# Kernel tuning notes

Hardware: AMD Instinct MI355X
Metric: run time of the kernel (lower is better)

The kernel has to match this reference:

```python
import jax, jax.numpy as jnp
import numpy as np

N_HEAD = 16
N_EMBD = 2048
HEAD_DIM = N_EMBD // N_HEAD


def setup_inputs() -> dict:
    key = jax.random.key(0)
    kx, kqkv, kp = jax.random.split(key, 3)
    B, S = 2, 2048
    x = jax.random.normal(kx, (B, S, N_EMBD), dtype=jnp.float32)
    # torch nn.Linear weights, stored as [out, in]; y = x @ W.T
    scale = 1.0 / np.sqrt(N_EMBD)
    Wqkv = jax.random.uniform(kqkv, (3 * N_EMBD, N_EMBD), dtype=jnp.float32, minval=-scale, maxval=scale)
    Wproj = jax.random.uniform(kp, (N_EMBD, N_EMBD), dtype=jnp.float32, minval=-scale, maxval=scale)
    return {"x": x, "Wqkv": Wqkv, "Wproj": Wproj}


def reference(x, Wqkv, Wproj):
    B, S, E = x.shape
    qkv = x @ Wqkv.T  # [B,S,3E]
    q, k, v = jnp.split(qkv, 3, axis=2)
    # [B,H,S,D]
    q = q.reshape(B, S, N_HEAD, HEAD_DIM).transpose(0, 2, 1, 3)
    k = k.reshape(B, S, N_HEAD, HEAD_DIM).transpose(0, 2, 1, 3)
    v = v.reshape(B, S, N_HEAD, HEAD_DIM).transpose(0, 2, 1, 3)
    scores = jnp.einsum('bhqd,bhkd->bhqk', q, k) / jnp.sqrt(jnp.float32(HEAD_DIM))
    causal = jnp.tril(jnp.ones((S, S), dtype=bool))  # [S,S]
    scores = jnp.where(causal[None, None, :, :], scores, -jnp.inf)
    weights = jax.nn.softmax(scores, axis=-1)
    out = jnp.einsum('bhqk,bhkd->bhqd', weights, v)  # [B,H,S,D]
    out = out.transpose(0, 2, 1, 3).reshape(B, S, E)
    return out @ Wproj.T
```

## Files before the change

### kernel.cpp

```cpp
#include <hip/hip_runtime.h>
#include <cstdint>
#include <cstddef>

typedef __bf16 bf16;
typedef __bf16 bf16x8 __attribute__((ext_vector_type(8)));
typedef float  f32x4  __attribute__((ext_vector_type(4)));

static_assert(sizeof(bf16x8) == 16, "bf16x8 must be 16B");

__device__ __forceinline__ void async_copy16(const bf16* g, bf16* l) {
  __builtin_amdgcn_global_load_lds(
      (__attribute__((address_space(1))) void*)(g),
      (__attribute__((address_space(3))) void*)(l),
      16, 0, 0);
}

__global__ __launch_bounds__(256)
void conv_f32_bf16(const float* __restrict__ s, bf16* __restrict__ d) {
  const size_t i = ((size_t)blockIdx.x * 256 + threadIdx.x) * 8;
  const f32x4 a = *(const f32x4*)(s + i);
  const f32x4 b = *(const f32x4*)(s + i + 4);
  bf16x8 o;
#pragma unroll
  for (int e = 0; e < 4; ++e) { o[e] = (bf16)a[e]; o[4 + e] = (bf16)b[e]; }
  *(bf16x8*)(d + i) = o;
}

template<int AMODE, int CMODE>
__global__ __launch_bounds__(256, 2)
void gemm_bt(const bf16* __restrict__ A, const bf16* __restrict__ W,
             float* __restrict__ Crow, bf16* __restrict__ Cq,
             bf16* __restrict__ Ck, bf16* __restrict__ Cvt,
             int M, int N, int K, int nbase) {
  __shared__ bf16 As[128 * 64];
  __shared__ bf16 Ws[128 * 64];

  const int tid  = threadIdx.x;
  const int wave = tid >> 6;
  const int lane = tid & 63;
  const int quad = lane >> 4;
  const int r    = lane & 15;
  const int m0 = blockIdx.y * 128;
  const int n0 = blockIdx.x * 128;
  const int wm = (wave >> 1) * 64;
  const int wn = (wave & 1) * 64;

  const int lrow   = lane >> 3;
  const int gchunk = (lane & 7) ^ lrow;

  f32x4 acc[4][4] = {};

  for (int k0 = 0; k0 < K; k0 += 64) {
    __syncthreads();
    for (int j = 0; j < 4; ++j) {
      const int rbase = (wave * 4 + j) * 8;
      const int rowA  = m0 + rbase + lrow;
      const bf16* aSrc;
      if constexpr (AMODE == 2) {
        const int b = rowA >> 11, s = rowA & 2047;
        aSrc = A + ((size_t)(b * 16 + (k0 >> 7)) * 2048 + s) * 128
                 + (k0 & 127) + gchunk * 8;
      } else {
        aSrc = A + (size_t)rowA * K + k0 + gchunk * 8;
      }
      async_copy16(aSrc, As + rbase * 64);
      async_copy16(W + (size_t)(n0 + rbase + lrow) * K + k0 + gchunk * 8,
                   Ws + rbase * 64);
    }
    __syncthreads();
    for (int ks = 0; ks < 2; ++ks) {
      bf16x8 af[4], bfv[4];
      for (int i = 0; i < 4; ++i) {
        const int ar = wm + i * 16 + r;
        af[i]  = *(const bf16x8*)(As + ar * 64 + (((ks * 4 + quad) ^ (ar & 7)) * 8));
        const int br = wn + i * 16 + r;
        bfv[i] = *(const bf16x8*)(Ws + br * 64 + (((ks * 4 + quad) ^ (br & 7)) * 8));
      }
      for (int i = 0; i < 4; ++i)
        for (int j = 0; j < 4; ++j)
          acc[i][j] = __builtin_amdgcn_mfma_f32_16x16x32_bf16(af[i], bfv[j], acc[i][j], 0, 0, 0);
    }
  }

  for (int i = 0; i < 4; ++i) {
    const int growb = m0 + wm + i * 16 + quad * 4;
    for (int j = 0; j < 4; ++j) {
      const int gcol = n0 + wn + j * 16 + r;
      for (int rg = 0; rg < 4; ++rg) {
        const int grow = growb + rg;
        if constexpr (CMODE == 1) {
          const int gc = nbase + gcol;
          const int which = gc >> 11;
          const int h = (gc >> 7) & 15;
          const int d = gc & 127;
          const int b = grow >> 11;
          const int s = grow & 2047;
          const bf16 v = (bf16)acc[i][j][rg];
          if (which == 0)
            Cq[(((size_t)b * 16 + h) * 2048 + s) * 128 + d] = v;
          else if (which == 1)
            Ck[(((size_t)b * 16 + h) * 2048 + s) * 128 + d] = v;
          else
            Cvt[(((size_t)b * 16 + h) * 128 + d) * 2048 + s] = v;
        } else {
          Crow[(size_t)grow * N + gcol] = acc[i][j][rg];
        }
      }
    }
  }
}

__global__ __launch_bounds__(256, 2)
void attn_kernel(bf16* __restrict__ Q, const bf16* __restrict__ K,
                 const bf16* __restrict__ Vt, int S) {
  __shared__ bf16 k_lds[64 * 128];
  __shared__ bf16 v_lds[128 * 64];
  __shared__ bf16 p_lds[4][32 * 64];

  const int tid = threadIdx.x, wave = tid >> 6, lane = tid & 63;
  const int quad = lane >> 4, r = lane & 15;
  const int bh = blockIdx.y;
  const int q0 = (gridDim.x - 1 - blockIdx.x) * 128;
  const int qrow0 = q0 + wave * 32;
  bf16* Qh = Q + (size_t)bh * S * 128;
  const bf16* Kh = K + (size_t)bh * S * 128;
  const bf16* Vth = Vt + (size_t)bh * 128 * S;

  bf16x8 qf[2][4];
  for (int mt = 0; mt < 2; ++mt)
    for (int ks = 0; ks < 4; ++ks)
      qf[mt][ks] = *(const bf16x8*)(Qh + (size_t)(qrow0 + mt * 16 + r) * 128 + ks * 32 + quad * 8);

  f32x4 o_acc[2][8] = {};
  f32x4 m_run[2], l_run[2];
  for (int mt = 0; mt < 2; ++mt)
    for (int t = 0; t < 4; ++t) { m_run[mt][t] = -1e30f; l_run[mt][t] = 0.f; }

  const float sc = 0.0883883476483184f * 1.4426950408889634f;
  const int nkv = (q0 + 128) >> 6;

  for (int kt = 0; kt < nkv; ++kt) {
    const int kv0 = kt << 6;
    __syncthreads();
    for (int j = 0; j < 4; ++j) {
      const int lin = j * 256 + tid;
      const int row = lin >> 4;
      const int ch  = lin & 15;
      *(bf16x8*)(k_lds + row * 128 + (ch ^ (row & 7)) * 8) =
          *(const bf16x8*)(Kh + (size_t)(kv0 + row) * 128 + ch * 8);
    }
    for (int j = 0; j < 4; ++j) {
      const int lin = j * 256 + tid;
      const int row = lin >> 3;
      const int c   = lin & 7;
      *(bf16x8*)(v_lds + row * 64 + (c ^ (row & 7)) * 8) =
          *(const bf16x8*)(Vth + (size_t)row * S + kv0 + c * 8);
    }
    __syncthreads();

    if (kv0 <= qrow0 + 31) {
      f32x4 sa[2][4] = {};
      for (int ks = 0; ks < 4; ++ks) {
        bf16x8 kf[4];
        for (int nt = 0; nt < 4; ++nt) {
          const int kr = nt * 16 + r;
          kf[nt] = *(const bf16x8*)(k_lds + kr * 128 + (((ks * 4 + quad) ^ (kr & 7)) * 8));
        }
        for (int mt = 0; mt < 2; ++mt)
          for (int nt = 0; nt < 4; ++nt)
            sa[mt][nt] = __builtin_amdgcn_mfma_f32_16x16x32_bf16(qf[mt][ks], kf[nt], sa[mt][nt], 0, 0, 0);
      }
      if (kv0 + 63 > qrow0) {
        for (int mt = 0; mt < 2; ++mt)
          for (int nt = 0; nt < 4; ++nt) {
            const int col  = kv0 + nt * 16 + r;
            const int rowb = qrow0 + mt * 16 + quad * 4;
            for (int rg = 0; rg < 4; ++rg)
              if (col > rowb + rg) sa[mt][nt][rg] = -1e30f;
          }
      }
      for (int mt = 0; mt < 2; ++mt) {
        f32x4 mx = sa[mt][0];
        for (int nt = 1; nt < 4; ++nt)
          for (int rg = 0; rg < 4; ++rg) mx[rg] = fmaxf(mx[rg], sa[mt][nt][rg]);
        for (int off = 1; off < 16; off <<= 1)
          for (int rg = 0; rg < 4; ++rg) mx[rg] = fmaxf(mx[rg], __shfl_xor(mx[rg], off, 64));
        f32x4 alpha;
        for (int rg = 0; rg < 4; ++rg) {
          const float mnew = fmaxf(m_run[mt][rg], mx[rg]);
          alpha[rg] = exp2f((m_run[mt][rg] - mnew) * sc);
          m_run[mt][rg] = mnew;
        }
        f32x4 rsum = {0.f, 0.f, 0.f, 0.f};
        for (int nt = 0; nt < 4; ++nt)
          for (int rg = 0; rg < 4; ++rg) {
            const float p = exp2f((sa[mt][nt][rg] - m_run[mt][rg]) * sc);
            sa[mt][nt][rg] = p;
            rsum[rg] += p;
          }
        for (int off = 1; off < 16; off <<= 1)
          for (int rg = 0; rg < 4; ++rg) rsum[rg] += __shfl_xor(rsum[rg], off, 64);
        for (int rg = 0; rg < 4; ++rg) l_run[mt][rg] = l_run[mt][rg] * alpha[rg] + rsum[rg];
        for (int nt2 = 0; nt2 < 8; ++nt2)
          for (int rg = 0; rg < 4; ++rg) o_acc[mt][nt2][rg] *= alpha[rg];
        for (int nt = 0; nt < 4; ++nt)
          for (int rg = 0; rg < 4; ++rg) {
            const int prow = mt * 16 + quad * 4 + rg;
            const int pcol = nt * 16 + r;
            p_lds[wave][prow * 64 + (((pcol >> 3) ^ (prow & 7)) * 8) + (pcol & 7)] =
                (bf16)sa[mt][nt][rg];
          }
      }
      for (int ks2 = 0; ks2 < 2; ++ks2) {
        bf16x8 pf[2];
        for (int mt = 0; mt < 2; ++mt) {
          const int prow = mt * 16 + r;
          pf[mt] = *(const bf16x8*)(p_lds[wave] + prow * 64 + (((ks2 * 4 + quad) ^ (prow & 7)) * 8));
        }
        for (int nt2 = 0; nt2 < 8; ++nt2) {
          const int vrow = nt2 * 16 + r;
          const bf16x8 vf = *(const bf16x8*)(v_lds + vrow * 64 + (((ks2 * 4 + quad) ^ (vrow & 7)) * 8));
          for (int mt = 0; mt < 2; ++mt)
            o_acc[mt][nt2] = __builtin_amdgcn_mfma_f32_16x16x32_bf16(pf[mt], vf, o_acc[mt][nt2], 0, 0, 0);
        }
      }
    }
  }

  for (int mt = 0; mt < 2; ++mt) {
    f32x4 inv;
    for (int rg = 0; rg < 4; ++rg) inv[rg] = 1.0f / l_run[mt][rg];
    for (int nt2 = 0; nt2 < 8; ++nt2) {
      const int d = nt2 * 16 + r;
      for (int rg = 0; rg < 4; ++rg) {
        const int s = qrow0 + mt * 16 + quad * 4 + rg;
        Qh[(size_t)s * 128 + d] = (bf16)(o_acc[mt][nt2][rg] * inv[rg]);
      }
    }
  }
}

extern "C" void kernel_launch(void* const* d_in, const int* in_sizes, int n_in,
                              void* d_out, int out_size, void* d_ws, size_t ws_size,
                              hipStream_t stream) {
  const float* x     = (const float*)d_in[0];
  const float* Wqkv  = (const float*)d_in[1];
  const float* Wproj = (const float*)d_in[2];
  float* out = (float*)d_out;

  const int Bm = 4096, E = 2048;
  const size_t plane = 8388608;

  bf16* qw  = (bf16*)d_ws;
  bf16* vtw = qw + plane;
  bf16* xb  = vtw + plane;
  bf16* kw  = (bf16*)d_out;
  bf16* wqb = kw + plane;

  conv_f32_bf16<<<8388608 / 2048, 256, 0, stream>>>(x, xb);
  conv_f32_bf16<<<6291456 / 2048, 256, 0, stream>>>(Wqkv, wqb);
  gemm_bt<0, 1><<<dim3(3072 / 128, Bm / 128), 256, 0, stream>>>(
      xb, wqb, nullptr, qw, kw, vtw, Bm, 3072, E, 0);
  conv_f32_bf16<<<6291456 / 2048, 256, 0, stream>>>(Wqkv + 6291456, wqb);
  gemm_bt<0, 1><<<dim3(3072 / 128, Bm / 128), 256, 0, stream>>>(
      xb, wqb, nullptr, qw, kw, vtw, Bm, 3072, E, 3072);
  attn_kernel<<<dim3(2048 / 128, 32), 256, 0, stream>>>(qw, kw, vtw, 2048);
  conv_f32_bf16<<<4194304 / 2048, 256, 0, stream>>>(Wproj, xb);
  gemm_bt<2, 0><<<dim3(2048 / 128, Bm / 128), 256, 0, stream>>>(
      qw, xb, out, nullptr, nullptr, nullptr, Bm, 2048, E, 0);
}
```

Before: 443.2 us.

## Shrink attention query tile to 64 rows, one 16-row MFMA tile per wave

The attention kernel now processes 64 query rows per block instead of 128, with each wave owning a single 16-row tile. This halves per-wave accumulator registers, allows a launch bound of four blocks per CU, doubles the grid and gives finer causal load balance. The cost is that each K/V tile staged in LDS is reused by half as many query rows, which roughly doubles K/V global loads and LDS staging per unit of work.

```diff
diff --git a/kernel.cpp b/kernel.cpp
--- a/kernel.cpp
+++ b/kernel.cpp
@@ -110,34 +110,32 @@
   }
 }
 
-__global__ __launch_bounds__(256, 2)
+__global__ __launch_bounds__(256, 4)
 void attn_kernel(bf16* __restrict__ Q, const bf16* __restrict__ K,
                  const bf16* __restrict__ Vt, int S) {
   __shared__ bf16 k_lds[64 * 128];
   __shared__ bf16 v_lds[128 * 64];
-  __shared__ bf16 p_lds[4][32 * 64];
+  __shared__ bf16 p_lds[4][16 * 64];
 
   const int tid = threadIdx.x, wave = tid >> 6, lane = tid & 63;
   const int quad = lane >> 4, r = lane & 15;
   const int bh = blockIdx.y;
-  const int q0 = (gridDim.x - 1 - blockIdx.x) * 128;
-  const int qrow0 = q0 + wave * 32;
+  const int q0 = (gridDim.x - 1 - blockIdx.x) * 64;
+  const int qrow0 = q0 + wave * 16;
   bf16* Qh = Q + (size_t)bh * S * 128;
   const bf16* Kh = K + (size_t)bh * S * 128;
   const bf16* Vth = Vt + (size_t)bh * 128 * S;
 
-  bf16x8 qf[2][4];
-  for (int mt = 0; mt < 2; ++mt)
-    for (int ks = 0; ks < 4; ++ks)
-      qf[mt][ks] = *(const bf16x8*)(Qh + (size_t)(qrow0 + mt * 16 + r) * 128 + ks * 32 + quad * 8);
-
-  f32x4 o_acc[2][8] = {};
-  f32x4 m_run[2], l_run[2];
-  for (int mt = 0; mt < 2; ++mt)
-    for (int t = 0; t < 4; ++t) { m_run[mt][t] = -1e30f; l_run[mt][t] = 0.f; }
+  bf16x8 qf[4];
+  for (int ks = 0; ks < 4; ++ks)
+    qf[ks] = *(const bf16x8*)(Qh + (size_t)(qrow0 + r) * 128 + ks * 32 + quad * 8);
+
+  f32x4 o_acc[8] = {};
+  f32x4 m_run, l_run;
+  for (int t = 0; t < 4; ++t) { m_run[t] = -1e30f; l_run[t] = 0.f; }
 
   const float sc = 0.0883883476483184f * 1.4426950408889634f;
-  const int nkv = (q0 + 128) >> 6;
+  const int nkv = (q0 + 64) >> 6;
 
   for (int kt = 0; kt < nkv; ++kt) {
     const int kv0 = kt << 6;
@@ -158,84 +156,73 @@
     }
     __syncthreads();
 
-    if (kv0 <= qrow0 + 31) {
-      f32x4 sa[2][4] = {};
-      for (int ks = 0; ks < 4; ++ks) {
-        bf16x8 kf[4];
-        for (int nt = 0; nt < 4; ++nt) {
-          const int kr = nt * 16 + r;
-          kf[nt] = *(const bf16x8*)(k_lds + kr * 128 + (((ks * 4 + quad) ^ (kr & 7)) * 8));
+    f32x4 sa[4] = {};
+    for (int ks = 0; ks < 4; ++ks) {
+      bf16x8 kf[4];
+      for (int nt = 0; nt < 4; ++nt) {
+        const int kr = nt * 16 + r;
+        kf[nt] = *(const bf16x8*)(k_lds + kr * 128 + (((ks * 4 + quad) ^ (kr & 7)) * 8));
+      }
+      for (int nt = 0; nt < 4; ++nt)
+        sa[nt] = __builtin_amdgcn_mfma_f32_16x16x32_bf16(qf[ks], kf[nt], sa[nt], 0, 0, 0);
+    }
+    if (kv0 + 63 > qrow0) {
+      for (int nt = 0; nt < 4; ++nt) {
+        const int col  = kv0 + nt * 16 + r;
+        const int rowb = qrow0 + quad * 4;
+        for (int rg = 0; rg < 4; ++rg)
+          if (col > rowb + rg) sa[nt][rg] = -1e30f;
+      }
+    }
+    {
+      f32x4 mx = sa[0];
+      for (int nt = 1; nt < 4; ++nt)
+        for (int rg = 0; rg < 4; ++rg) mx[rg] = fmaxf(mx[rg], sa[nt][rg]);
+      for (int off = 1; off < 16; off <<= 1)
+        for (int rg = 0; rg < 4; ++rg) mx[rg] = fmaxf(mx[rg], __shfl_xor(mx[rg], off, 64));
+      f32x4 alpha;
+      for (int rg = 0; rg < 4; ++rg) {
+        const float mnew = fmaxf(m_run[rg], mx[rg]);
+        alpha[rg] = exp2f((m_run[rg] - mnew) * sc);
+        m_run[rg] = mnew;
+      }
+      f32x4 rsum = {0.f, 0.f, 0.f, 0.f};
+      for (int nt = 0; nt < 4; ++nt)
+        for (int rg = 0; rg < 4; ++rg) {
+          const float p = exp2f((sa[nt][rg] - m_run[rg]) * sc);
+          sa[nt][rg] = p;
+          rsum[rg] += p;
         }
-        for (int mt = 0; mt < 2; ++mt)
-          for (int nt = 0; nt < 4; ++nt)
-            sa[mt][nt] = __builtin_amdgcn_mfma_f32_16x16x32_bf16(qf[mt][ks], kf[nt], sa[mt][nt], 0, 0, 0);
-      }
-      if (kv0 + 63 > qrow0) {
-        for (int mt = 0; mt < 2; ++mt)
-          for (int nt = 0; nt < 4; ++nt) {
-            const int col  = kv0 + nt * 16 + r;
-            const int rowb = qrow0 + mt * 16 + quad * 4;
-            for (int rg = 0; rg < 4; ++rg)
-              if (col > rowb + rg) sa[mt][nt][rg] = -1e30f;
-          }
-      }
-      for (int mt = 0; mt < 2; ++mt) {
-        f32x4 mx = sa[mt][0];
-        for (int nt = 1; nt < 4; ++nt)
-          for (int rg = 0; rg < 4; ++rg) mx[rg] = fmaxf(mx[rg], sa[mt][nt][rg]);
-        for (int off = 1; off < 16; off <<= 1)
-          for (int rg = 0; rg < 4; ++rg) mx[rg] = fmaxf(mx[rg], __shfl_xor(mx[rg], off, 64));
-        f32x4 alpha;
+      for (int off = 1; off < 16; off <<= 1)
+        for (int rg = 0; rg < 4; ++rg) rsum[rg] += __shfl_xor(rsum[rg], off, 64);
+      for (int rg = 0; rg < 4; ++rg) l_run[rg] = l_run[rg] * alpha[rg] + rsum[rg];
+      for (int nt2 = 0; nt2 < 8; ++nt2)
+        for (int rg = 0; rg < 4; ++rg) o_acc[nt2][rg] *= alpha[rg];
+      for (int nt = 0; nt < 4; ++nt)
         for (int rg = 0; rg < 4; ++rg) {
-          const float mnew = fmaxf(m_run[mt][rg], mx[rg]);
-          alpha[rg] = exp2f((m_run[mt][rg] - mnew) * sc);
-          m_run[mt][rg] = mnew;
+          const int prow = quad * 4 + rg;
+          const int pcol = nt * 16 + r;
+          p_lds[wave][prow * 64 + (((pcol >> 3) ^ (prow & 7)) * 8) + (pcol & 7)] =
+              (bf16)sa[nt][rg];
         }
-        f32x4 rsum = {0.f, 0.f, 0.f, 0.f};
-        for (int nt = 0; nt < 4; ++nt)
-          for (int rg = 0; rg < 4; ++rg) {
-            const float p = exp2f((sa[mt][nt][rg] - m_run[mt][rg]) * sc);
-            sa[mt][nt][rg] = p;
-            rsum[rg] += p;
-          }
-        for (int off = 1; off < 16; off <<= 1)
-          for (int rg = 0; rg < 4; ++rg) rsum[rg] += __shfl_xor(rsum[rg], off, 64);
-        for (int rg = 0; rg < 4; ++rg) l_run[mt][rg] = l_run[mt][rg] * alpha[rg] + rsum[rg];
-        for (int nt2 = 0; nt2 < 8; ++nt2)
-          for (int rg = 0; rg < 4; ++rg) o_acc[mt][nt2][rg] *= alpha[rg];
-        for (int nt = 0; nt < 4; ++nt)
-          for (int rg = 0; rg < 4; ++rg) {
-            const int prow = mt * 16 + quad * 4 + rg;
-            const int pcol = nt * 16 + r;
-            p_lds[wave][prow * 64 + (((pcol >> 3) ^ (prow & 7)) * 8) + (pcol & 7)] =
-                (bf16)sa[mt][nt][rg];
-          }
-      }
-      for (int ks2 = 0; ks2 < 2; ++ks2) {
-        bf16x8 pf[2];
-        for (int mt = 0; mt < 2; ++mt) {
-          const int prow = mt * 16 + r;
-          pf[mt] = *(const bf16x8*)(p_lds[wave] + prow * 64 + (((ks2 * 4 + quad) ^ (prow & 7)) * 8));
-        }
-        for (int nt2 = 0; nt2 < 8; ++nt2) {
-          const int vrow = nt2 * 16 + r;
-          const bf16x8 vf = *(const bf16x8*)(v_lds + vrow * 64 + (((ks2 * 4 + quad) ^ (vrow & 7)) * 8));
-          for (int mt = 0; mt < 2; ++mt)
-            o_acc[mt][nt2] = __builtin_amdgcn_mfma_f32_16x16x32_bf16(pf[mt], vf, o_acc[mt][nt2], 0, 0, 0);
-        }
-      }
-    }
-  }
-
-  for (int mt = 0; mt < 2; ++mt) {
-    f32x4 inv;
-    for (int rg = 0; rg < 4; ++rg) inv[rg] = 1.0f / l_run[mt][rg];
-    for (int nt2 = 0; nt2 < 8; ++nt2) {
-      const int d = nt2 * 16 + r;
-      for (int rg = 0; rg < 4; ++rg) {
-        const int s = qrow0 + mt * 16 + quad * 4 + rg;
-        Qh[(size_t)s * 128 + d] = (bf16)(o_acc[mt][nt2][rg] * inv[rg]);
-      }
+    }
+    for (int ks2 = 0; ks2 < 2; ++ks2) {
+      const bf16x8 pf = *(const bf16x8*)(p_lds[wave] + r * 64 + (((ks2 * 4 + quad) ^ (r & 7)) * 8));
+      for (int nt2 = 0; nt2 < 8; ++nt2) {
+        const int vrow = nt2 * 16 + r;
+        const bf16x8 vf = *(const bf16x8*)(v_lds + vrow * 64 + (((ks2 * 4 + quad) ^ (vrow & 7)) * 8));
+        o_acc[nt2] = __builtin_amdgcn_mfma_f32_16x16x32_bf16(pf, vf, o_acc[nt2], 0, 0, 0);
+      }
+    }
+  }
+
+  f32x4 inv;
+  for (int rg = 0; rg < 4; ++rg) inv[rg] = 1.0f / l_run[rg];
+  for (int nt2 = 0; nt2 < 8; ++nt2) {
+    const int d = nt2 * 16 + r;
+    for (int rg = 0; rg < 4; ++rg) {
+      const int s = qrow0 + quad * 4 + rg;
+      Qh[(size_t)s * 128 + d] = (bf16)(o_acc[nt2][rg] * inv[rg]);
     }
   }
 }
@@ -264,7 +251,7 @@
   conv_f32_bf16<<<6291456 / 2048, 256, 0, stream>>>(Wqkv + 6291456, wqb);
   gemm_bt<0, 1><<<dim3(3072 / 128, Bm / 128), 256, 0, stream>>>(
       xb, wqb, nullptr, qw, kw, vtw, Bm, 3072, E, 3072);
-  attn_kernel<<<dim3(2048 / 128, 32), 256, 0, stream>>>(qw, kw, vtw, 2048);
+  attn_kernel<<<dim3(2048 / 64, 32), 256, 0, stream>>>(qw, kw, vtw, 2048);
   conv_f32_bf16<<<4194304 / 2048, 256, 0, stream>>>(Wproj, xb);
   gemm_bt<2, 0><<<dim3(2048 / 128, Bm / 128), 256, 0, stream>>>(
       qw, xb, out, nullptr, nullptr, nullptr, Bm, 2048, E, 0);
```

Measured after the change: 592.7 us. 1.34x slower.

## Double-buffer K/V tiles with async global-to-LDS copies in attention

Applied to the files above, without the earlier changes.

Replaces the synchronous register-staged K and V tile loads with `global_load_lds` async copies into double-buffered LDS. The next tile is prefetched while the current one is computed on, and one of the two barriers per iteration is dropped. K is split into two 64-column halves with a lane-based XOR swizzle, and the P scratch swizzle gains an extra row-bit term to reduce bank conflicts. LDS use grows to about 80 KB per block, which may constrain occupancy. Correctness depends on the barrier also waiting for the async copies to land.

```diff
diff --git a/kernel.cpp b/kernel.cpp
--- a/kernel.cpp
+++ b/kernel.cpp
@@ -113,12 +113,14 @@
 __global__ __launch_bounds__(256, 2)
 void attn_kernel(bf16* __restrict__ Q, const bf16* __restrict__ K,
                  const bf16* __restrict__ Vt, int S) {
-  __shared__ bf16 k_lds[64 * 128];
-  __shared__ bf16 v_lds[128 * 64];
-  __shared__ bf16 p_lds[4][32 * 64];
+  __shared__ bf16 k_lds[2 * 2 * 64 * 64];
+  __shared__ bf16 v_lds[2 * 128 * 64];
+  __shared__ bf16 p_lds[4 * 32 * 64];
 
   const int tid = threadIdx.x, wave = tid >> 6, lane = tid & 63;
   const int quad = lane >> 4, r = lane & 15;
+  const int lrow = lane >> 3;
+  const int gchunk = (lane & 7) ^ lrow;
   const int bh = blockIdx.y;
   const int q0 = (gridDim.x - 1 - blockIdx.x) * 128;
   const int qrow0 = q0 + wave * 32;
@@ -139,32 +141,36 @@
   const float sc = 0.0883883476483184f * 1.4426950408889634f;
   const int nkv = (q0 + 128) >> 6;
 
+  auto stage_tile = [&](int kv0, int buf) {
+#pragma unroll
+    for (int t = 0; t < 4; ++t) {
+      const int id = wave * 4 + t;
+      const int rg = id >> 1, half = id & 1;
+      async_copy16(Kh + (size_t)(kv0 + rg * 8 + lrow) * 128 + half * 64 + gchunk * 8,
+                   k_lds + buf * 8192 + half * 4096 + rg * 512);
+      const int rgv = wave * 4 + t;
+      async_copy16(Vth + (size_t)(rgv * 8 + lrow) * S + kv0 + gchunk * 8,
+                   v_lds + buf * 8192 + rgv * 512);
+    }
+  };
+
+  stage_tile(0, 0);
+
   for (int kt = 0; kt < nkv; ++kt) {
     const int kv0 = kt << 6;
     __syncthreads();
-    for (int j = 0; j < 4; ++j) {
-      const int lin = j * 256 + tid;
-      const int row = lin >> 4;
-      const int ch  = lin & 15;
-      *(bf16x8*)(k_lds + row * 128 + (ch ^ (row & 7)) * 8) =
-          *(const bf16x8*)(Kh + (size_t)(kv0 + row) * 128 + ch * 8);
-    }
-    for (int j = 0; j < 4; ++j) {
-      const int lin = j * 256 + tid;
-      const int row = lin >> 3;
-      const int c   = lin & 7;
-      *(bf16x8*)(v_lds + row * 64 + (c ^ (row & 7)) * 8) =
-          *(const bf16x8*)(Vth + (size_t)row * S + kv0 + c * 8);
-    }
-    __syncthreads();
+    if (kt + 1 < nkv) stage_tile((kt + 1) << 6, (kt + 1) & 1);
+    const int bo = (kt & 1) * 8192;
 
     if (kv0 <= qrow0 + 31) {
       f32x4 sa[2][4] = {};
       for (int ks = 0; ks < 4; ++ks) {
+        const int idx = ks * 4 + quad;
+        const int half = idx >> 3, cg = idx & 7;
         bf16x8 kf[4];
         for (int nt = 0; nt < 4; ++nt) {
           const int kr = nt * 16 + r;
-          kf[nt] = *(const bf16x8*)(k_lds + kr * 128 + (((ks * 4 + quad) ^ (kr & 7)) * 8));
+          kf[nt] = *(const bf16x8*)(k_lds + bo + half * 4096 + kr * 64 + ((cg ^ (r & 7)) * 8));
         }
         for (int mt = 0; mt < 2; ++mt)
           for (int nt = 0; nt < 4; ++nt)
@@ -207,19 +213,21 @@
           for (int rg = 0; rg < 4; ++rg) {
             const int prow = mt * 16 + quad * 4 + rg;
             const int pcol = nt * 16 + r;
-            p_lds[wave][prow * 64 + (((pcol >> 3) ^ (prow & 7)) * 8) + (pcol & 7)] =
-                (bf16)sa[mt][nt][rg];
+            const int swz = ((pcol >> 3) ^ (prow & 7) ^ ((prow >> 3) & 1));
+            p_lds[wave * 2048 + prow * 64 + swz * 8 + (pcol & 7)] = (bf16)sa[mt][nt][rg];
           }
       }
       for (int ks2 = 0; ks2 < 2; ++ks2) {
+        const int cc = ks2 * 4 + quad;
         bf16x8 pf[2];
         for (int mt = 0; mt < 2; ++mt) {
           const int prow = mt * 16 + r;
-          pf[mt] = *(const bf16x8*)(p_lds[wave] + prow * 64 + (((ks2 * 4 + quad) ^ (prow & 7)) * 8));
+          const int swz = (cc ^ (prow & 7) ^ ((prow >> 3) & 1));
+          pf[mt] = *(const bf16x8*)(p_lds + wave * 2048 + prow * 64 + swz * 8);
         }
         for (int nt2 = 0; nt2 < 8; ++nt2) {
           const int vrow = nt2 * 16 + r;
-          const bf16x8 vf = *(const bf16x8*)(v_lds + vrow * 64 + (((ks2 * 4 + quad) ^ (vrow & 7)) * 8));
+          const bf16x8 vf = *(const bf16x8*)(v_lds + bo + vrow * 64 + ((cc ^ (r & 7)) * 8));
           for (int mt = 0; mt < 2; ++mt)
             o_acc[mt][nt2] = __builtin_amdgcn_mfma_f32_16x16x32_bf16(pf[mt], vf, o_acc[mt][nt2], 0, 0, 0);
         }
```

Result: slower. 452.1 us (+2.0%).
